# Kernel optimization log

Measured on AMD Instinct MI355X. Metric: run time of the kernel, lower is better.

The kernel has to match this reference:

```python
import jax, jax.numpy as jnp
import numpy as np

B, L, HID = 2, 2048, 2048
H, KVH, HD = 8, 1, 256
GROUPS = H // KVH
THETA = 10000.0
NEG_INF = -1e9


def _rope_cos_sin(seq_len, hd):
    inv_freq = 1.0 / (THETA ** (jnp.arange(0, hd, 2, dtype=jnp.float32) / hd))
    t = jnp.arange(seq_len, dtype=jnp.float32)
    freqs = jnp.outer(t, inv_freq)                # [L, hd/2]
    emb = jnp.concatenate([freqs, freqs], axis=-1)  # [L, hd]
    return jnp.cos(emb), jnp.sin(emb)


def _rotate_half(x):
    x1, x2 = jnp.split(x, 2, axis=-1)
    return jnp.concatenate([-x2, x1], axis=-1)


def _apply_rope(x, cos, sin):
    # x: [B, h, L, hd]; cos/sin: [L, hd] broadcast over batch/heads
    return x * cos[None, None] + _rotate_half(x) * sin[None, None]


def setup_inputs() -> dict:
    key = jax.random.key(0)
    kx, kq, kk, kv, ko = jax.random.split(key, 5)
    s = lambda fan_in: 1.0 / np.sqrt(fan_in)
    x = jax.random.normal(kx, (B, L, HID), dtype=jnp.float32)
    Wq = jax.random.normal(kq, (HID, H * HD), dtype=jnp.float32) * s(HID)
    Wk = jax.random.normal(kk, (HID, KVH * HD), dtype=jnp.float32) * s(HID)
    Wv = jax.random.normal(kv, (HID, KVH * HD), dtype=jnp.float32) * s(HID)
    Wo = jax.random.normal(ko, (H * HD, HID), dtype=jnp.float32) * s(H * HD)
    # causal additive mask, same semantics as SDPA attn_mask (float, additive)
    causal = jnp.tril(jnp.ones((L, L), dtype=bool))
    mask = jnp.where(causal, 0.0, NEG_INF).astype(jnp.float32)[None, None]
    return {"x": x, "Wq": Wq, "Wk": Wk, "Wv": Wv, "Wo": Wo, "mask": mask}


def reference(x, Wq, Wk, Wv, Wo, mask):
    # projections -> [B, h, L, hd]
    q = (x @ Wq).reshape(B, L, H, HD).transpose(0, 2, 1, 3)
    k = (x @ Wk).reshape(B, L, KVH, HD).transpose(0, 2, 1, 3)
    v = (x @ Wv).reshape(B, L, KVH, HD).transpose(0, 2, 1, 3)
    cos, sin = _rope_cos_sin(L, HD)
    q = _apply_rope(q, cos, sin)
    k = _apply_rope(k, cos, sin)
    # GQA: replicate kv heads (repeat_interleave over head dim)
    k = jnp.repeat(k, GROUPS, axis=1)
    v = jnp.repeat(v, GROUPS, axis=1)
    scale = HD ** -0.5
    scores = jnp.einsum("bhqd,bhkd->bhqk", q, k) * scale + mask
    attn = jax.nn.softmax(scores.astype(jnp.float32), axis=-1).astype(q.dtype)
    out = jnp.einsum("bhqk,bhkd->bhqd", attn, v)
    out = out.transpose(0, 2, 1, 3).reshape(B, L, H * HD)
    return out @ Wo
```

## Files before the change

kernel.cpp:

```cpp
#include <hip/hip_runtime.h>

typedef unsigned short u16;
typedef __attribute__((ext_vector_type(8))) short short8x;
typedef __attribute__((ext_vector_type(4))) float f32x4;

#define B_ 2
#define L_ 2048
#define HID_ 2048
#define H_ 8
#define HD_ 256

__device__ __forceinline__ u16 f2bf(float f) {
  union { float f; unsigned u; } v; v.f = f;
  unsigned r = v.u + 0x7FFFu + ((v.u >> 16) & 1u);
  return (u16)(r >> 16);
}
__device__ __forceinline__ float bf2f(u16 u) {
  union { unsigned u; float f; } v; v.u = ((unsigned)u) << 16;
  return v.f;
}

__device__ __forceinline__ void gload_lds16(const void* g, void* l) {
  __builtin_amdgcn_global_load_lds((const __attribute__((address_space(1))) unsigned*)g,
                                   (__attribute__((address_space(3))) unsigned*)l, 16, 0, 0);
}

__global__ __launch_bounds__(256) void cvt_x_kernel(const float4* __restrict__ in,
                                                    u16* __restrict__ out) {
  int idx = blockIdx.x * 256 + threadIdx.x;
  float4 v = in[idx];
  u16* o = out + (size_t)idx * 4;
  o[0] = f2bf(v.x); o[1] = f2bf(v.y); o[2] = f2bf(v.z); o[3] = f2bf(v.w);
}

__global__ __launch_bounds__(256) void cvt_wt_kernel(const float* __restrict__ W,
                                                     u16* __restrict__ Wt, int K, int N) {
  __shared__ float tile[32][33];
  int n0 = blockIdx.x * 32, k0 = blockIdx.y * 32;
  int tx = threadIdx.x, ty = threadIdx.y;
#pragma unroll
  for (int i = 0; i < 32; i += 8)
    tile[ty + i][tx] = W[(size_t)(k0 + ty + i) * N + n0 + tx];
  __syncthreads();
#pragma unroll
  for (int i = 0; i < 32; i += 8)
    Wt[(size_t)(n0 + ty + i) * K + k0 + tx] = f2bf(tile[tx][ty + i]);
}

__global__ __launch_bounds__(256) void rope_kernel(const u16* __restrict__ in,
                                                   u16* __restrict__ out, int nh_shift,
                                                   int in_stride, int in_off, float scale) {
  int idx = blockIdx.x * 256 + threadIdx.x;
  int nh = 1 << nh_shift;
  int d = idx & 127;
  int t = idx >> 7;
  int h = t & (nh - 1);
  int row = t >> nh_shift;
  int l = row & (L_ - 1);
  int b = row >> 11;
  size_t ibase = (size_t)row * in_stride + in_off + h * 256 + d;
  float x1 = bf2f(in[ibase]);
  float x2 = bf2f(in[ibase + 128]);
  float f = exp2f(-(float)d * (13.287712379549449f / 128.0f));
  float ang = (float)l * f;
  float s, c;
  sincosf(ang, &s, &c);
  size_t obase = ((size_t)(b * nh + h) * L_ + l) * 256 + d;
  out[obase] = f2bf((x1 * c - x2 * s) * scale);
  out[obase + 128] = f2bf((x2 * c + x1 * s) * scale);
}

__global__ __launch_bounds__(256) void vt_kernel(const u16* __restrict__ qkvproj,
                                                 u16* __restrict__ vt) {
  int idx = blockIdx.x * 256 + threadIdx.x;
  int l = idx & 2047;
  int d = (idx >> 11) & 255;
  int b = idx >> 19;
  vt[idx] = qkvproj[((size_t)b * 2048 + l) * 2560 + 2304 + d];
}

template <int F32OUT>
__global__ __launch_bounds__(256) void gemm_bt_kernel(const u16* __restrict__ A,
                                                      const u16* __restrict__ Bt,
                                                      void* __restrict__ Cv,
                                                      int M, int N, int K) {
  __shared__ __attribute__((aligned(16))) u16 As[128 * 32];
  __shared__ __attribute__((aligned(16))) u16 Bs[128 * 32];
  const int tid = threadIdx.x;
  const int lane = tid & 63;
  const int w = tid >> 6;
  const int wr = w >> 1, wc = w & 1;
  const int nbx = gridDim.x;
  int flat = blockIdx.y * nbx + blockIdx.x;
  int nwg = nbx * gridDim.y;
  int q8 = nwg >> 3, r8 = nwg & 7;
  int xcd = flat & 7, idx8 = flat >> 3;
  int neu = (xcd < r8 ? xcd * (q8 + 1) : r8 * (q8 + 1) + (xcd - r8) * q8) + idx8;
  const int m0 = (neu / nbx) * 128, n0 = (neu % nbx) * 128;
  const int l15 = lane & 15, l4 = lane >> 4;
  f32x4 acc[4][4] = {};
  for (int kt = 0; kt < K; kt += 32) {
#pragma unroll
    for (int i = 0; i < 2; ++i) {
      int c = tid + i * 256;
      int row = c >> 2, cin = c & 3;
      gload_lds16(A + (size_t)(m0 + row) * K + kt + cin * 8,
                  (char*)As + (i * 256 + w * 64) * 16);
      gload_lds16(Bt + (size_t)(n0 + row) * K + kt + cin * 8,
                  (char*)Bs + (i * 256 + w * 64) * 16);
    }
    __syncthreads();
    short8x a[4], b[4];
#pragma unroll
    for (int m = 0; m < 4; ++m)
      a[m] = *(const short8x*)(&As[(wr * 64 + m * 16 + l15) * 32 + l4 * 8]);
#pragma unroll
    for (int n = 0; n < 4; ++n)
      b[n] = *(const short8x*)(&Bs[(wc * 64 + n * 16 + l15) * 32 + l4 * 8]);
#pragma unroll
    for (int m = 0; m < 4; ++m)
#pragma unroll
      for (int n = 0; n < 4; ++n)
        acc[m][n] = __builtin_amdgcn_mfma_f32_16x16x32_bf16(a[m], b[n], acc[m][n], 0, 0, 0);
    __syncthreads();
  }
#pragma unroll
  for (int m = 0; m < 4; ++m) {
#pragma unroll
    for (int n = 0; n < 4; ++n) {
      int gcol = n0 + wc * 64 + n * 16 + l15;
#pragma unroll
      for (int r = 0; r < 4; ++r) {
        int grow = m0 + wr * 64 + m * 16 + l4 * 4 + r;
        if (F32OUT)
          ((float*)Cv)[(size_t)grow * N + gcol] = acc[m][n][r];
        else
          ((u16*)Cv)[(size_t)grow * N + gcol] = f2bf(acc[m][n][r]);
      }
    }
  }
}

__global__ __launch_bounds__(256) void flash_kernel(const u16* __restrict__ qb,
                                                    const u16* __restrict__ kb,
                                                    const u16* __restrict__ vt,
                                                    u16* __restrict__ attn_o) {
  __shared__ __attribute__((aligned(16))) u16 Kbuf[64 * 256];
  __shared__ __attribute__((aligned(16))) u16 Vbuf[256 * 64];
  __shared__ __attribute__((aligned(16))) u16 Ps[4 * 16 * 64];
  const int x = blockIdx.x;
  const int j = 31 - (x >> 4);
  const int bh = x & 15;
  const int b = bh >> 3;
  const int h = bh & 7;
  const int tid = threadIdx.x, lane = tid & 63, w = tid >> 6;
  const int l15 = lane & 15, l4 = lane >> 4;
  const int q0 = j * 64 + w * 16;
  const int nt = j + 1;

  const u16* qrow = qb + ((size_t)(b * 8 + h) * L_ + q0 + l15) * 256;
  short8x qf[8];
#pragma unroll
  for (int kc = 0; kc < 8; ++kc)
    qf[kc] = *(const short8x*)(qrow + kc * 32 + l4 * 8);

  f32x4 o[16] = {};
  float mrow = -3e38f, srow = 0.f;

  const u16* kbase = kb + (size_t)b * (L_ * 256);
  const u16* vbase = vt + (size_t)b * (256 * L_);

  for (int t = 0; t < nt; ++t) {
#pragma unroll
    for (int i2 = 0; i2 < 8; ++i2) {
      int c = i2 * 256 + tid;
      int rk = c >> 5, cck = c & 31, jk = cck ^ (rk & 7);
      gload_lds16(kbase + (size_t)(t * 64 + rk) * 256 + jk * 8,
                  (char*)Kbuf + (i2 * 256 + w * 64) * 16);
      int rd = c >> 3, ccv = c & 7, jv = ccv ^ (rd & 7);
      gload_lds16(vbase + (size_t)rd * L_ + t * 64 + jv * 8,
                  (char*)Vbuf + (i2 * 256 + w * 64) * 16);
    }
    asm volatile("s_waitcnt vmcnt(0)" ::: "memory");
    __syncthreads();

    f32x4 sacc[4] = {};
    __builtin_amdgcn_s_setprio(1);
#pragma unroll
    for (int kc = 0; kc < 8; ++kc)
#pragma unroll
      for (int n = 0; n < 4; ++n) {
        int row = n * 16 + l15;
        short8x kf = *(const short8x*)((const char*)Kbuf +
            ((row * 512 + kc * 64 + l4 * 16) ^ ((row & 7) << 4)));
        sacc[n] = __builtin_amdgcn_mfma_f32_16x16x32_bf16(kf, qf[kc], sacc[n], 0, 0, 0);
      }
    __builtin_amdgcn_s_setprio(0);
    float p[4][4];
    const bool dm = (t == j);
    const int qg = q0 + l15;
    float pm = -3e38f;
#pragma unroll
    for (int n = 0; n < 4; ++n)
#pragma unroll
      for (int r = 0; r < 4; ++r) {
        int kvg = t * 64 + n * 16 + l4 * 4 + r;
        float v = sacc[n][r];
        if (dm && (kvg > qg)) v = -1e30f;
        p[n][r] = v;
        pm = fmaxf(pm, v);
      }
    pm = fmaxf(pm, __shfl_xor(pm, 16));
    pm = fmaxf(pm, __shfl_xor(pm, 32));
    const bool defer = __all(pm <= mrow + 8.f);
    float mn, alpha;
    if (defer) {
      mn = mrow;
    } else {
      mn = fmaxf(mrow, pm);
      alpha = __expf(mrow - mn);
      mrow = mn;
    }
    float rs = 0.f;
#pragma unroll
    for (int n = 0; n < 4; ++n)
#pragma unroll
      for (int r = 0; r < 4; ++r) {
        p[n][r] = __expf(p[n][r] - mn);
        rs += p[n][r];
      }
    rs += __shfl_xor(rs, 16);
    rs += __shfl_xor(rs, 32);
    if (defer) {
      srow += rs;
    } else {
      srow = srow * alpha + rs;
      float av[4];
#pragma unroll
      for (int r = 0; r < 4; ++r)
        av[r] = __shfl(alpha, l4 * 4 + r, 16);
#pragma unroll
      for (int ff = 0; ff < 16; ++ff) {
        o[ff][0] *= av[0]; o[ff][1] *= av[1];
        o[ff][2] *= av[2]; o[ff][3] *= av[3];
      }
    }
#pragma unroll
    for (int n = 0; n < 4; ++n)
#pragma unroll
      for (int r = 0; r < 4; r += 2) {
        unsigned pk;
        asm("v_cvt_pk_bf16_f32 %0, %1, %2" : "=v"(pk) : "v"(p[n][r]), "v"(p[n][r + 1]));
        *(unsigned*)((char*)Ps + w * 2048 +
                     ((l15 * 128 + (n * 16 + l4 * 4 + r) * 2) ^ ((l15 & 7) << 4))) = pk;
      }
    asm volatile("s_waitcnt lgkmcnt(0)" ::: "memory");
    short8x paf[2];
#pragma unroll
    for (int kc2 = 0; kc2 < 2; ++kc2)
      paf[kc2] = *(const short8x*)((const char*)Ps + w * 2048 +
          ((l15 * 128 + kc2 * 64 + l4 * 16) ^ ((l15 & 7) << 4)));
    __builtin_amdgcn_s_setprio(1);
#pragma unroll
    for (int kc2 = 0; kc2 < 2; ++kc2)
#pragma unroll
      for (int ff = 0; ff < 16; ++ff) {
        int rd = ff * 16 + l15;
        short8x vf = *(const short8x*)((const char*)Vbuf +
            ((rd * 128 + kc2 * 64 + l4 * 16) ^ ((rd & 7) << 4)));
        o[ff] = __builtin_amdgcn_mfma_f32_16x16x32_bf16(paf[kc2], vf, o[ff], 0, 0, 0);
      }
    __builtin_amdgcn_s_setprio(0);
    __syncthreads();
  }
  float sv[4];
#pragma unroll
  for (int r = 0; r < 4; ++r)
    sv[r] = __shfl(srow, l4 * 4 + r, 16);
#pragma unroll
  for (int r = 0; r < 4; ++r) {
    float inv = 1.0f / sv[r];
    int grow = q0 + l4 * 4 + r;
    size_t base = ((size_t)b * L_ + grow) * (size_t)(H_ * HD_) + h * 256;
#pragma unroll
    for (int ff = 0; ff < 16; ++ff)
      attn_o[base + ff * 16 + l15] = f2bf(o[ff][r] * inv);
  }
}

extern "C" void kernel_launch(void* const* d_in, const int* in_sizes, int n_in,
                              void* d_out, int out_size, void* d_ws, size_t ws_size,
                              hipStream_t stream) {
  const float* x  = (const float*)d_in[0];
  const float* Wq = (const float*)d_in[1];
  const float* Wk = (const float*)d_in[2];
  const float* Wv = (const float*)d_in[3];
  const float* Wo = (const float*)d_in[4];
  float* out = (float*)d_out;
  char* ws = (char*)d_ws;
  size_t off = 0;
  auto alloc = [&](size_t bytes) {
    void* p = ws + off;
    off = (off + bytes + 255) & ~(size_t)255;
    return p;
  };
  u16* wqkv_t  = (u16*)alloc(2560ull * 2048 * 2);
  u16* wo_t    = (u16*)alloc(2048ull * 2048 * 2);
  u16* xbf     = (u16*)alloc(4096ull * 2048 * 2);
  u16* qkvproj = (u16*)alloc(4096ull * 2560 * 2);
  u16* kb      = (u16*)alloc(4096ull * 256 * 2);
  u16* vtb     = (u16*)alloc(4096ull * 256 * 2);
  u16* qbuf    = xbf;
  u16* attn_o  = qkvproj;

  cvt_x_kernel<<<8192, 256, 0, stream>>>((const float4*)x, xbf);
  cvt_wt_kernel<<<dim3(64, 64), dim3(32, 8), 0, stream>>>(Wq, wqkv_t, 2048, 2048);
  cvt_wt_kernel<<<dim3(8, 64),  dim3(32, 8), 0, stream>>>(Wk, wqkv_t + 2048ull * 2048, 2048, 256);
  cvt_wt_kernel<<<dim3(8, 64),  dim3(32, 8), 0, stream>>>(Wv, wqkv_t + 2304ull * 2048, 2048, 256);
  cvt_wt_kernel<<<dim3(64, 64), dim3(32, 8), 0, stream>>>(Wo, wo_t, 2048, 2048);

  gemm_bt_kernel<0><<<dim3(20, 32), 256, 0, stream>>>(xbf, wqkv_t, qkvproj, 4096, 2560, 2048);

  rope_kernel<<<16384, 256, 0, stream>>>(qkvproj, qbuf, 3, 2560, 0, 0.0625f);
  rope_kernel<<<2048, 256, 0, stream>>>(qkvproj, kb, 0, 2560, 2048, 1.0f);
  vt_kernel<<<4096, 256, 0, stream>>>(qkvproj, vtb);

  flash_kernel<<<512, 256, 0, stream>>>(qbuf, kb, vtb, attn_o);

  gemm_bt_kernel<1><<<dim3(16, 32), 256, 0, stream>>>(attn_o, wo_t, out, 4096, 2048, 2048);
}
```

Baseline: 262.6 us.

## Double-buffer K/V tiles in flash attention to overlap loads with compute

The flash attention kernel now keeps two LDS buffers each for K and V. It prefetches the next KV tile with async global-to-LDS loads while the current tile goes through QK^T, softmax and PV. This is meant to hide global memory latency behind the MFMA work instead of stalling on vmcnt(0) at the start of every tile. In exchange, LDS use roughly doubles to about 136KB per block, which may cut occupancy to one block per CU.

```diff
diff --git a/kernel.cpp b/kernel.cpp
--- a/kernel.cpp
+++ b/kernel.cpp
@@ -145,8 +145,8 @@
                                                     const u16* __restrict__ kb,
                                                     const u16* __restrict__ vt,
                                                     u16* __restrict__ attn_o) {
-  __shared__ __attribute__((aligned(16))) u16 Kbuf[64 * 256];
-  __shared__ __attribute__((aligned(16))) u16 Vbuf[256 * 64];
+  __shared__ __attribute__((aligned(16))) u16 Kbuf[2][64 * 256];
+  __shared__ __attribute__((aligned(16))) u16 Vbuf[2][256 * 64];
   __shared__ __attribute__((aligned(16))) u16 Ps[4 * 16 * 64];
   const int x = blockIdx.x;
   const int j = 31 - (x >> 4);
@@ -170,19 +170,27 @@
   const u16* kbase = kb + (size_t)b * (L_ * 256);
   const u16* vbase = vt + (size_t)b * (256 * L_);
 
+#define STAGE(t, s)                                                            \
+  {                                                                            \
+    _Pragma("unroll") for (int i2 = 0; i2 < 8; ++i2) {                         \
+      int c = i2 * 256 + tid;                                                  \
+      int rk = c >> 5, cck = c & 31, jk = cck ^ (rk & 7);                      \
+      gload_lds16(kbase + (size_t)((t) * 64 + rk) * 256 + jk * 8,              \
+                  (char*)&Kbuf[s][0] + (i2 * 256 + w * 64) * 16);              \
+      int rd = c >> 3, ccv = c & 7, jv = ccv ^ (rd & 7);                       \
+      gload_lds16(vbase + (size_t)rd * L_ + (t) * 64 + jv * 8,                 \
+                  (char*)&Vbuf[s][0] + (i2 * 256 + w * 64) * 16);              \
+    }                                                                          \
+  }
+
+  STAGE(0, 0);
+  asm volatile("s_waitcnt vmcnt(0)" ::: "memory");
+  __syncthreads();
+
   for (int t = 0; t < nt; ++t) {
-#pragma unroll
-    for (int i2 = 0; i2 < 8; ++i2) {
-      int c = i2 * 256 + tid;
-      int rk = c >> 5, cck = c & 31, jk = cck ^ (rk & 7);
-      gload_lds16(kbase + (size_t)(t * 64 + rk) * 256 + jk * 8,
-                  (char*)Kbuf + (i2 * 256 + w * 64) * 16);
-      int rd = c >> 3, ccv = c & 7, jv = ccv ^ (rd & 7);
-      gload_lds16(vbase + (size_t)rd * L_ + t * 64 + jv * 8,
-                  (char*)Vbuf + (i2 * 256 + w * 64) * 16);
-    }
-    asm volatile("s_waitcnt vmcnt(0)" ::: "memory");
-    __syncthreads();
+    if (t + 1 < nt) STAGE(t + 1, (t + 1) & 1);
+    const char* Kb = (const char*)&Kbuf[t & 1][0];
+    const char* Vb = (const char*)&Vbuf[t & 1][0];
 
     f32x4 sacc[4] = {};
     __builtin_amdgcn_s_setprio(1);
@@ -191,7 +199,7 @@
 #pragma unroll
       for (int n = 0; n < 4; ++n) {
         int row = n * 16 + l15;
-        short8x kf = *(const short8x*)((const char*)Kbuf +
+        short8x kf = *(const short8x*)(Kb +
             ((row * 512 + kc * 64 + l4 * 16) ^ ((row & 7) << 4)));
         sacc[n] = __builtin_amdgcn_mfma_f32_16x16x32_bf16(kf, qf[kc], sacc[n], 0, 0, 0);
       }
@@ -266,11 +274,12 @@
 #pragma unroll
       for (int ff = 0; ff < 16; ++ff) {
         int rd = ff * 16 + l15;
-        short8x vf = *(const short8x*)((const char*)Vbuf +
+        short8x vf = *(const short8x*)(Vb +
             ((rd * 128 + kc2 * 64 + l4 * 16) ^ ((rd & 7) << 4)));
         o[ff] = __builtin_amdgcn_mfma_f32_16x16x32_bf16(paf[kc2], vf, o[ff], 0, 0, 0);
       }
     __builtin_amdgcn_s_setprio(0);
+    asm volatile("s_waitcnt vmcnt(0)" ::: "memory");
     __syncthreads();
   }
   float sv[4];
@@ -286,6 +295,7 @@
     for (int ff = 0; ff < 16; ++ff)
       attn_o[base + ff * 16 + l15] = f2bf(o[ff][r] * inv);
   }
+#undef STAGE
 }
 
 extern "C" void kernel_launch(void* const* d_in, const int* in_sizes, int n_in,
```

Result: faster. 255.1 us (-2.8%).
